# Performance work log

Hardware: AMD Instinct MI355X
Metric: run time of the kernel (lower is better)

## Reference

```python
import jax, jax.numpy as jnp
import numpy as np


def setup_inputs() -> dict:
    key = jax.random.key(0)
    k1, k2 = jax.random.split(key)
    x = jax.random.normal(k1, (64, 64, 112, 112), dtype=jnp.float32)
    weight = jax.random.normal(k2, (64, 64, 3, 3), dtype=jnp.float32) * 0.1
    alpha = jnp.ones((64, 1, 1), dtype=jnp.float32)
    return {"x": x, "weight": weight, "alpha": alpha}


def reference(x, weight, alpha):
    # Eval-mode forward of Conv2d_XnorPP_SCA:
    #   binarize activations with sign, ternarize weights with round(tanh(w)),
    #   standard conv2d (stride=1, padding=1, no bias), then per-out-channel alpha scale.
    x_bin = jnp.sign(x)                                  # [N, Cin, H, W]
    w_tern = jnp.round(jnp.tanh(weight))                 # [Cout, Cin, k, k], values in {-1, 0, 1}
    out = jax.lax.conv_general_dilated(
        x_bin, w_tern,
        window_strides=(1, 1),
        padding=((1, 1), (1, 1)),
        dimension_numbers=("NCHW", "OIHW", "NCHW"),
    )                                                    # [N, Cout, H, W]
    return out * alpha                                   # alpha [Cout,1,1] broadcasts over NCHW
```

## Files before the change

### kernel.cpp

```cpp
#include <hip/hip_runtime.h>
#include <math.h>

#define NB   64
#define CIN  64
#define COUT 64
#define HH   112
#define WW   112
#define KH   3
#define KW   3
#define MAXE (CIN*KH*KW)

__global__ void ternarize_compact_kernel(const float* __restrict__ w,
                                         int* __restrict__ nnz,
                                         int* __restrict__ entries) {
    __shared__ int cnt;
    const int co = blockIdx.x;
    if (threadIdx.x == 0) cnt = 0;
    __syncthreads();

    const int t  = threadIdx.x;
    const int ci = t / 9;
    const int r  = t - ci * 9;
    const int kh = r / 3;
    const int kw = r - kh * 3;

    const float wv = w[((co * CIN + ci) * KH + kh) * KW + kw];
    const int tv = (int)rintf(tanhf(wv));

    if (tv != 0) {
        const int idx = atomicAdd(&cnt, 1);
        int packed = (ci << 4) | (kh << 2) | kw;
        if (tv < 0) packed |= (int)0x80000000;
        entries[co * MAXE + idx] = packed;
    }
    __syncthreads();
    if (threadIdx.x == 0) nnz[co] = cnt;
}

__global__ void __launch_bounds__(256)
sparse_tern_conv_kernel(const float* __restrict__ x,
                        const float* __restrict__ alpha,
                        const int* __restrict__ nnz,
                        const int* __restrict__ entries,
                        float* __restrict__ out) {
    const int i  = blockIdx.x * 256 + threadIdx.x;
    const int w4 = i % 28;
    int t        = i / 28;
    const int h  = t % HH;
    t            = t / HH;
    const int co = t % COUT;
    const int n  = t / COUT;
    const int w0 = w4 * 4;

    const int cnt = nnz[co];
    float a0 = 0.f, a1 = 0.f, a2 = 0.f, a3 = 0.f;

    if (cnt > 0) {
        const float* __restrict__ xn = x + (size_t)n * (CIN * HH * WW);
        const int*   __restrict__ ep = entries + co * MAXE;
        for (int e = 0; e < cnt; ++e) {
            const int p  = ep[e];
            const float s = (p < 0) ? -1.f : 1.f;
            const int q  = p & 0x7fffffff;
            const int ci = q >> 4;
            const int kh = (q >> 2) & 3;
            const int kw = q & 3;
            const int hy = h + kh - 1;
            if ((unsigned)hy >= (unsigned)HH) continue;
            const float* __restrict__ row = xn + (ci * HH + hy) * WW;
            const int wx = w0 + kw - 1;
            #pragma unroll
            for (int j = 0; j < 4; ++j) {
                const int wj = wx + j;
                if ((unsigned)wj < (unsigned)WW) {
                    const float xv = row[wj];
                    const float sg = (xv > 0.f) ? 1.f : ((xv < 0.f) ? -1.f : 0.f);
                    const float c  = s * sg;
                    if (j == 0) a0 += c;
                    else if (j == 1) a1 += c;
                    else if (j == 2) a2 += c;
                    else a3 += c;
                }
            }
        }
    }

    const float al = alpha[co];
    float4 o;
    o.x = a0 * al; o.y = a1 * al; o.z = a2 * al; o.w = a3 * al;
    reinterpret_cast<float4*>(out)[i] = o;
}

extern "C" void kernel_launch(void* const* d_in, const int* in_sizes, int n_in,
                              void* d_out, int out_size, void* d_ws, size_t ws_size,
                              hipStream_t stream) {
    const float* x      = (const float*)d_in[0];
    const float* weight = (const float*)d_in[1];
    const float* alpha  = (const float*)d_in[2];
    float*       out    = (float*)d_out;

    int* nnz     = (int*)d_ws;
    int* entries = nnz + COUT;

    ternarize_compact_kernel<<<COUT, MAXE, 0, stream>>>(weight, nnz, entries);

    const int total4 = NB * COUT * HH * (WW / 4);
    sparse_tern_conv_kernel<<<total4 / 256, 256, 0, stream>>>(x, alpha, nnz, entries, out);
}
```

Measured before the change: 292.3 us.

## Fuse weight ternarization into conv kernel with per-block LDS entry list

Merges the separate weight-ternarize/compact kernel into the conv kernel. Each block now recomputes its output channel's compacted nonzero list into shared memory, and co moves to blockIdx.y. This removes a kernel launch and the global reads of the entry list, and gives uniform LDS reads for entries. Output is written with nontemporal vector stores. The cost is redundant tanh over 576 weights in every block plus an extra barrier, and the atomic ordering makes the accumulation order nondeterministic.

```diff
diff --git a/kernel.cpp b/kernel.cpp
--- a/kernel.cpp
+++ b/kernel.cpp
@@ -6,61 +6,61 @@
 #define COUT 64
 #define HH   112
 #define WW   112
-#define KH   3
-#define KW   3
-#define MAXE (CIN*KH*KW)
+#define W4   (WW/4)
+#define MAXE (CIN*3*3)
+#define PIX_PER_CO (NB*HH*W4)
 
-__global__ void ternarize_compact_kernel(const float* __restrict__ w,
-                                         int* __restrict__ nnz,
-                                         int* __restrict__ entries) {
+typedef float vfloat4 __attribute__((ext_vector_type(4)));
+
+__global__ void __launch_bounds__(256)
+fused_xnor_conv_kernel(const float* __restrict__ x,
+                       const float* __restrict__ w,
+                       const float* __restrict__ alpha,
+                       float* __restrict__ out) {
     __shared__ int cnt;
-    const int co = blockIdx.x;
+    __shared__ int entries[MAXE];
+
+    const int co = blockIdx.y;
+
     if (threadIdx.x == 0) cnt = 0;
     __syncthreads();
 
-    const int t  = threadIdx.x;
-    const int ci = t / 9;
-    const int r  = t - ci * 9;
-    const int kh = r / 3;
-    const int kw = r - kh * 3;
-
-    const float wv = w[((co * CIN + ci) * KH + kh) * KW + kw];
-    const int tv = (int)rintf(tanhf(wv));
-
-    if (tv != 0) {
-        const int idx = atomicAdd(&cnt, 1);
-        int packed = (ci << 4) | (kh << 2) | kw;
-        if (tv < 0) packed |= (int)0x80000000;
-        entries[co * MAXE + idx] = packed;
+    const float* __restrict__ wc = w + co * MAXE;
+    #pragma unroll
+    for (int s = 0; s < 3; ++s) {
+        const int t = threadIdx.x + s * 256;
+        if (t < MAXE) {
+            const float wv = wc[t];
+            const int tv = (int)rintf(tanhf(wv));
+            if (tv != 0) {
+                const int idx = atomicAdd(&cnt, 1);
+                const int ci = t / 9;
+                const int r  = t - ci * 9;
+                const int kh = r / 3;
+                const int kw = r - kh * 3;
+                int packed = (ci << 4) | (kh << 2) | kw;
+                if (tv < 0) packed |= (int)0x80000000;
+                entries[idx] = packed;
+            }
+        }
     }
     __syncthreads();
-    if (threadIdx.x == 0) nnz[co] = cnt;
-}
+    const int nn = cnt;
 
-__global__ void __launch_bounds__(256)
-sparse_tern_conv_kernel(const float* __restrict__ x,
-                        const float* __restrict__ alpha,
-                        const int* __restrict__ nnz,
-                        const int* __restrict__ entries,
-                        float* __restrict__ out) {
     const int i  = blockIdx.x * 256 + threadIdx.x;
-    const int w4 = i % 28;
-    int t        = i / 28;
-    const int h  = t % HH;
-    t            = t / HH;
-    const int co = t % COUT;
-    const int n  = t / COUT;
-    const int w0 = w4 * 4;
+    const int wq = i % W4;
+    int t2       = i / W4;
+    const int h  = t2 % HH;
+    const int n  = t2 / HH;
+    const int w0 = wq * 4;
 
-    const int cnt = nnz[co];
     float a0 = 0.f, a1 = 0.f, a2 = 0.f, a3 = 0.f;
 
-    if (cnt > 0) {
+    if (nn > 0) {
         const float* __restrict__ xn = x + (size_t)n * (CIN * HH * WW);
-        const int*   __restrict__ ep = entries + co * MAXE;
-        for (int e = 0; e < cnt; ++e) {
-            const int p  = ep[e];
-            const float s = (p < 0) ? -1.f : 1.f;
+        for (int e = 0; e < nn; ++e) {
+            const int p  = entries[e];
+            const float sgn = (p < 0) ? -1.f : 1.f;
             const int q  = p & 0x7fffffff;
             const int ci = q >> 4;
             const int kh = (q >> 2) & 3;
@@ -75,7 +75,7 @@
                 if ((unsigned)wj < (unsigned)WW) {
                     const float xv = row[wj];
                     const float sg = (xv > 0.f) ? 1.f : ((xv < 0.f) ? -1.f : 0.f);
-                    const float c  = s * sg;
+                    const float c  = sgn * sg;
                     if (j == 0) a0 += c;
                     else if (j == 1) a1 += c;
                     else if (j == 2) a2 += c;
@@ -86,9 +86,12 @@
     }
 
     const float al = alpha[co];
-    float4 o;
+    vfloat4 o;
     o.x = a0 * al; o.y = a1 * al; o.z = a2 * al; o.w = a3 * al;
-    reinterpret_cast<float4*>(out)[i] = o;
+
+    vfloat4* dst = reinterpret_cast<vfloat4*>(
+        out + ((((size_t)n * COUT + co) * HH + h) * WW + w0));
+    __builtin_nontemporal_store(o, dst);
 }
 
 extern "C" void kernel_launch(void* const* d_in, const int* in_sizes, int n_in,
@@ -99,11 +102,6 @@
     const float* alpha  = (const float*)d_in[2];
     float*       out    = (float*)d_out;
 
-    int* nnz     = (int*)d_ws;
-    int* entries = nnz + COUT;
-
-    ternarize_compact_kernel<<<COUT, MAXE, 0, stream>>>(weight, nnz, entries);
-
-    const int total4 = NB * COUT * HH * (WW / 4);
-    sparse_tern_conv_kernel<<<total4 / 256, 256, 0, stream>>>(x, alpha, nnz, entries, out);
+    dim3 grid(PIX_PER_CO / 256, COUT);
+    fused_xnor_conv_kernel<<<grid, 256, 0, stream>>>(x, weight, alpha, out);
 }
```

Measured after the change: 333.1 us. +13.9%, slower.
